# Optimization experiments

Hardware: AMD Instinct MI355X
Metric: run time of the kernel (lower is better)

The kernel has to match this reference:

```python
import jax, jax.numpy as jnp
import numpy as np

N, IN, HID, OUT, HEADS, E = 50000, 256, 128, 128, 2, 800000
NEG_SLOPE = 0.2


def gat_conv(x, edge_src, edge_dst, W, att_src, att_dst, bias):
    # x: [N, F_in]; W: [F_in, H*C]; att_*: [H, C]; bias: [C]
    n = x.shape[0]
    H, C = att_src.shape
    xl = (x @ W).reshape(n, H, C)                       # [N, H, C]
    a_src = jnp.sum(xl * att_src, axis=-1)              # [N, H]
    a_dst = jnp.sum(xl * att_dst, axis=-1)              # [N, H]
    e = jax.nn.leaky_relu(a_src[edge_src] + a_dst[edge_dst], NEG_SLOPE)  # [E+N, H]
    e_max = jax.ops.segment_max(e, edge_dst, num_segments=n)            # [N, H]
    e = jnp.exp(e - e_max[edge_dst])
    denom = jax.ops.segment_sum(e, edge_dst, num_segments=n)            # [N, H]
    alpha = e / (denom[edge_dst] + 1e-16)                               # [E+N, H]
    msg = xl[edge_src] * alpha[:, :, None]                              # [E+N, H, C]
    out = jax.ops.segment_sum(msg, edge_dst, num_segments=n)            # [N, H, C]
    return out.mean(axis=1) + bias                                      # concat=False: head mean


def setup_inputs() -> dict:
    key = jax.random.key(0)
    ks = jax.random.split(key, 12)
    x = jax.random.normal(ks[0], (N, IN), dtype=jnp.float32)
    edge_index = jax.random.randint(ks[1], (2, E), 0, N, dtype=jnp.int64)
    s = 0.1
    W0 = jax.random.normal(ks[2], (IN, HEADS * HID), dtype=jnp.float32) * s
    att_src0 = jax.random.normal(ks[3], (HEADS, HID), dtype=jnp.float32) * s
    att_dst0 = jax.random.normal(ks[4], (HEADS, HID), dtype=jnp.float32) * s
    bias0 = jnp.zeros((HID,), dtype=jnp.float32)
    W1 = jax.random.normal(ks[5], (HID, HEADS * HID), dtype=jnp.float32) * s
    att_src1 = jax.random.normal(ks[6], (HEADS, HID), dtype=jnp.float32) * s
    att_dst1 = jax.random.normal(ks[7], (HEADS, HID), dtype=jnp.float32) * s
    bias1 = jnp.zeros((HID,), dtype=jnp.float32)
    proj_w = jax.random.normal(ks[8], (HID, OUT), dtype=jnp.float32) * s
    proj_b = jnp.zeros((OUT,), dtype=jnp.float32)
    return {"x": x, "edge_index": edge_index,
            "W0": W0, "att_src0": att_src0, "att_dst0": att_dst0, "bias0": bias0,
            "W1": W1, "att_src1": att_src1, "att_dst1": att_dst1, "bias1": bias1,
            "proj_w": proj_w, "proj_b": proj_b}


def reference(x, edge_index, W0, att_src0, att_dst0, bias0, W1, att_src1, att_dst1, bias1, proj_w, proj_b):
    n = x.shape[0]
    loops = jnp.arange(n, dtype=edge_index.dtype)
    # PyG GATConv default add_self_loops=True
    src = jnp.concatenate([edge_index[0], loops])
    dst = jnp.concatenate([edge_index[1], loops])
    h = gat_conv(x, src, dst, W0, att_src0, att_dst0, bias0)
    h = jax.nn.gelu(h, approximate=False)
    h = gat_conv(h, src, dst, W1, att_src1, att_dst1, bias1)
    h = jax.nn.gelu(h, approximate=False)
    return h @ proj_w + proj_b
```

## Files before the change

### kernel.cpp

```cpp
#include <hip/hip_runtime.h>
#include <hip/hip_fp16.h>
#include <math.h>


#define NEG_SLOPE 0.2f

typedef __attribute__((ext_vector_type(8))) _Float16 f16x8;
typedef __attribute__((ext_vector_type(8))) ushort u16x8;
typedef __attribute__((ext_vector_type(4))) float f32x4;

__device__ __forceinline__ ushort f32_to_f16u(float x)
{
    return __half_as_ushort(__float2half(x));
}

__device__ __forceinline__ float f16u_to_f32(ushort u)
{
    return __half2float(__ushort_as_half(u));
}

__device__ __forceinline__ void split_f16(float x, ushort& h, ushort& l)
{
    const __half hh = __float2half(x);
    h = __half_as_ushort(hh);
    l = __half_as_ushort(__float2half(x - __half2float(hh)));
}

__device__ __forceinline__ float lrelu(float x)
{
    return x > 0.f ? x : NEG_SLOPE * x;
}

__device__ __forceinline__ float gelu_exact(float x)
{
    return 0.5f * x * (1.0f + erff(x * 0.7071067811865476f));
}

__global__ __launch_bounds__(256)
void prep_kernel(const float* __restrict__ W0, const float* __restrict__ W1,
                 const float* __restrict__ PW,
                 const float* __restrict__ as0, const float* __restrict__ ad0,
                 const float* __restrict__ as1, const float* __restrict__ ad1,
                 ushort* __restrict__ w0h, ushort* __restrict__ w0l,
                 ushort* __restrict__ w1h, ushort* __restrict__ w1l,
                 ushort* __restrict__ pwh, ushort* __restrict__ pwl,
                 float* __restrict__ wtd0, float* __restrict__ wt1,
                 int* __restrict__ cnt, int N)
{
    const int blk = blockIdx.x;
    if (blk >= 577) {
        int t2 = (blk - 577) * 256 + threadIdx.x;
        if (t2 < N) cnt[t2] = 0;
        return;
    }
    if (blk == 576) {
        const int col = threadIdx.x;
        float4 o;
        if (col < 128) o = make_float4(as0[col], 0.f, ad0[col], 0.f);
        else           o = make_float4(0.f, as0[col], 0.f, ad0[col]);
        *(float4*)(wtd0 + col * 4) = o;
        return;
    }
    if (blk < 448) {
        int t = blk * 256 + threadIdx.x;
        ushort h, l;
        if (t < 65536) {
            int k = t >> 8, n = t & 255;
            split_f16(W0[t], h, l);
            w0h[n * 256 + k] = h; w0l[n * 256 + k] = l;
        } else if (t < 65536 + 32768) {
            int u = t - 65536;
            int k = u >> 8, n = u & 255;
            split_f16(W1[u], h, l);
            w1h[n * 128 + k] = h; w1l[n * 128 + k] = l;
        } else {
            int u = t - 65536 - 32768;
            int k = u >> 7, n = u & 127;
            split_f16(PW[u], h, l);
            pwh[n * 128 + k] = h; pwl[n * 128 + k] = l;
        }
        return;
    }
    const int k = blk - 448;
    const int t = threadIdx.x;
    const int h = t >> 7, c = t & 127;
    const int lane = t & 63, wid = t >> 6;
    const float w = W1[(size_t)k * 256 + h * 128 + c];
    float ps = w * as1[h * 128 + c];
    float pd = w * ad1[h * 128 + c];
#pragma unroll
    for (int off = 1; off < 64; off <<= 1) {
        ps += __shfl_xor(ps, off, 64);
        pd += __shfl_xor(pd, off, 64);
    }
    __shared__ float sm[4][2];
    if (lane == 0) { sm[wid][0] = ps; sm[wid][1] = pd; }
    __syncthreads();
    if (t == 0) {
        wt1[k * 4 + 0] = sm[0][0] + sm[1][0];
        wt1[k * 4 + 1] = sm[2][0] + sm[3][0];
        wt1[k * 4 + 2] = sm[0][1] + sm[1][1];
        wt1[k * 4 + 3] = sm[2][1] + sm[3][1];
    }
}

template<int BN, bool SPLITA>
__global__ __launch_bounds__(512)
void mfma_gemm3(const float* __restrict__ Af,
                const ushort* __restrict__ A16,
                const ushort* __restrict__ Bth, const ushort* __restrict__ Btl,
                const float* __restrict__ bias,
                float* __restrict__ Cf, ushort* __restrict__ Cb,
                const float* __restrict__ watt,
                float* __restrict__ a_sc, float* __restrict__ a_dc,
                int M, int K)
{
    constexpr int NF = BN / 64;
    __shared__ ushort Ah[4][128][8];
    __shared__ ushort Bh[4][BN][8];
    __shared__ ushort Bl[4][BN][8];

    const int tid = threadIdx.x;
    const int r0 = blockIdx.x * 128;
    const int w = tid >> 6, lane = tid & 63;
    const int wr = (w & 1) * 64;
    const int wc = (w >> 1) * (BN / 4);
    const int lr = lane & 15, kb = lane >> 4;

    const int arow = tid >> 2;
    const int apl = tid & 3;

    f32x4 acc[4][NF] = {};

    for (int kk = 0; kk < K; kk += 32) {
        {
            const int row = r0 + arow;
            u16x8 h0 = {};
            if (row < M) {
                if constexpr (SPLITA) {
                    const float* p = Af + (size_t)row * K + kk + apl * 8;
                    float4 v0 = *(const float4*)(p);
                    float4 v1 = *(const float4*)(p + 4);
                    h0[0] = f32_to_f16u(v0.x); h0[1] = f32_to_f16u(v0.y);
                    h0[2] = f32_to_f16u(v0.z); h0[3] = f32_to_f16u(v0.w);
                    h0[4] = f32_to_f16u(v1.x); h0[5] = f32_to_f16u(v1.y);
                    h0[6] = f32_to_f16u(v1.z); h0[7] = f32_to_f16u(v1.w);
                } else {
                    h0 = *(const u16x8*)(A16 + (size_t)row * K + kk + apl * 8);
                }
            }
            *(u16x8*)&Ah[apl][arow][0] = h0;
        }
        if constexpr (BN == 256) {
            const int col = tid >> 1, half = tid & 1;
            const ushort* ph = Bth + (size_t)col * K + kk + half * 16;
            const ushort* pl = Btl + (size_t)col * K + kk + half * 16;
            *(u16x8*)&Bh[half * 2 + 0][col][0] = *(const u16x8*)(ph);
            *(u16x8*)&Bh[half * 2 + 1][col][0] = *(const u16x8*)(ph + 8);
            *(u16x8*)&Bl[half * 2 + 0][col][0] = *(const u16x8*)(pl);
            *(u16x8*)&Bl[half * 2 + 1][col][0] = *(const u16x8*)(pl + 8);
        } else {
            const int col = tid >> 2, pl = tid & 3;
            *(u16x8*)&Bh[pl][col][0] = *(const u16x8*)(Bth + (size_t)col * K + kk + pl * 8);
            *(u16x8*)&Bl[pl][col][0] = *(const u16x8*)(Btl + (size_t)col * K + kk + pl * 8);
        }
        __syncthreads();

        f16x8 ah[4];
#pragma unroll
        for (int m = 0; m < 4; ++m)
            ah[m] = *(const f16x8*)&Ah[kb][wr + m * 16 + lr][0];
#pragma unroll
        for (int n = 0; n < NF; ++n) {
            const f16x8 bh = *(const f16x8*)&Bh[kb][wc + n * 16 + lr][0];
            const f16x8 bl = *(const f16x8*)&Bl[kb][wc + n * 16 + lr][0];
#pragma unroll
            for (int m = 0; m < 4; ++m) {
                acc[m][n] = __builtin_amdgcn_mfma_f32_16x16x32_f16(ah[m], bh, acc[m][n], 0, 0, 0);
                acc[m][n] = __builtin_amdgcn_mfma_f32_16x16x32_f16(ah[m], bl, acc[m][n], 0, 0, 0);
            }
        }
        __syncthreads();
    }

#pragma unroll
    for (int n = 0; n < NF; ++n) {
        const int col = wc + n * 16 + lr;
        const float bv = bias ? bias[col] : 0.f;
#pragma unroll
        for (int m = 0; m < 4; ++m) {
            const int rowb = r0 + wr + m * 16 + kb * 4;
#pragma unroll
            for (int j = 0; j < 4; ++j) {
                const int row = rowb + j;
                if (row < M) {
                    const float val = acc[m][n][j] + bv;
                    if (Cf) Cf[(size_t)row * BN + col] = val;
                    if (Cb) Cb[(size_t)row * BN + col] = f32_to_f16u(val);
                }
            }
        }
    }

    if (watt) {
        float* sp = (float*)&Ah[0][0][0];
        float4 wv[NF];
#pragma unroll
        for (int n = 0; n < NF; ++n)
            wv[n] = *(const float4*)(watt + (wc + n * 16 + lr) * 4);
#pragma unroll
        for (int m = 0; m < 4; ++m) {
#pragma unroll
            for (int j = 0; j < 4; ++j) {
                float s0 = 0.f, s1 = 0.f, s2 = 0.f, s3 = 0.f;
#pragma unroll
                for (int n = 0; n < NF; ++n) {
                    const float v = acc[m][n][j];
                    s0 += v * wv[n].x;
                    s1 += v * wv[n].y;
                    s2 += v * wv[n].z;
                    s3 += v * wv[n].w;
                }
#pragma unroll
                for (int off = 1; off < 16; off <<= 1) {
                    s0 += __shfl_xor(s0, off, 64);
                    s1 += __shfl_xor(s1, off, 64);
                    s2 += __shfl_xor(s2, off, 64);
                    s3 += __shfl_xor(s3, off, 64);
                }
                if (lr == 0) {
                    const int row = wr + m * 16 + kb * 4 + j;
                    float* d = sp + ((w >> 1) * 128 + row) * 4;
                    d[0] = s0; d[1] = s1; d[2] = s2; d[3] = s3;
                }
            }
        }
        __syncthreads();
        const int row = tid >> 2, comp = tid & 3;
        const float s = sp[(0 * 128 + row) * 4 + comp]
                      + sp[(1 * 128 + row) * 4 + comp]
                      + sp[(2 * 128 + row) * 4 + comp]
                      + sp[(3 * 128 + row) * 4 + comp];
        const int gr = r0 + row;
        if (gr < M) {
            if (comp < 2) a_sc[(size_t)gr * 2 + comp] = s;
            else          a_dc[(size_t)gr * 2 + (comp - 2)] = s;
        }
    }
}

__global__ __launch_bounds__(256)
void gat_gather_kernel(const ushort* __restrict__ xlb,
                       const int* __restrict__ rowptr,
                       const int* __restrict__ esrc,
                       const float* __restrict__ a_si,
                       const float* __restrict__ a_di,
                       const float* __restrict__ bias,
                       const float* __restrict__ watt,
                       float* __restrict__ a_so, float* __restrict__ a_do,
                       ushort* __restrict__ outh,
                       int n)
{
    const int wave = threadIdx.x >> 6;
    const int lane = threadIdx.x & 63;
    const int v = blockIdx.x * 4 + wave;
    if (v >= n) return;
    const int half = lane >> 5;
    const int il = lane & 31;
    const int ch8 = il << 3;
    const int hsel = il >> 4;

    const float2 advv = *(const float2*)(a_di + (size_t)v * 2);
    const float2 asvv = *(const float2*)(a_si + (size_t)v * 2);
    const float wself0 = __expf(lrelu(asvv.x + advv.x));
    const float wself1 = __expf(lrelu(asvv.y + advv.y));
    const float wselfh = hsel ? wself1 : wself0;

    const u16x8 xv = *(const u16x8*)(xlb + (size_t)v * 256 + ch8);
    float acc[8];
#pragma unroll
    for (int k = 0; k < 8; ++k)
        acc[k] = (half == 0) ? wselfh * f16u_to_f32(xv[k]) : 0.f;

    float ssum0 = (il == 0) ? wself0 : 0.f;
    float ssum1 = (il == 0) ? wself1 : 0.f;

    const int beg = rowptr[v], end = rowptr[v + 1];
    for (int i = beg; i < end; i += 32) {
        const int cnt = min(32, end - i);
        int myidx = 0;
        float myw0 = 0.f, myw1 = 0.f;
        if (il < cnt) {
            myidx = esrc[i + il];
            const float2 e = *(const float2*)(a_si + (size_t)myidx * 2);
            myw0 = __expf(lrelu(e.x + advv.x));
            myw1 = __expf(lrelu(e.y + advv.y));
        }
        ssum0 += myw0;
        ssum1 += myw1;
#pragma unroll 2
        for (int j = 0; j < cnt; j += 2) {
            const int jj = j + half;
            const int src = __shfl(myidx, jj, 32);
            const float w0 = __shfl(myw0, jj, 32);
            const float w1 = __shfl(myw1, jj, 32);
            const float wgt = hsel ? w1 : w0;
            const u16x8 xs = *(const u16x8*)(xlb + (size_t)src * 256 + ch8);
#pragma unroll
            for (int k = 0; k < 8; ++k)
                acc[k] += wgt * f16u_to_f32(xs[k]);
        }
    }

#pragma unroll
    for (int off = 1; off <= 16; off <<= 1) {
        ssum0 += __shfl_xor(ssum0, off, 64);
        ssum1 += __shfl_xor(ssum1, off, 64);
    }
    const float inv = 1.0f / ((hsel ? ssum1 : ssum0) + 1e-16f);

    float o[8];
#pragma unroll
    for (int k = 0; k < 8; ++k) {
        float a = acc[k] + __shfl_xor(acc[k], 32, 64);
        a *= inv;
        o[k] = 0.5f * (a + __shfl_xor(a, 16, 64));
    }

    if (il < 16) {
        const float4 bb0 = *(const float4*)(bias + ch8);
        const float4 bb1 = *(const float4*)(bias + ch8 + 4);
        o[0] = gelu_exact(o[0] + bb0.x);
        o[1] = gelu_exact(o[1] + bb0.y);
        o[2] = gelu_exact(o[2] + bb0.z);
        o[3] = gelu_exact(o[3] + bb0.w);
        o[4] = gelu_exact(o[4] + bb1.x);
        o[5] = gelu_exact(o[5] + bb1.y);
        o[6] = gelu_exact(o[6] + bb1.z);
        o[7] = gelu_exact(o[7] + bb1.w);

        if (watt) {
            float s0 = 0.f, s1 = 0.f, d0 = 0.f, d1 = 0.f;
#pragma unroll
            for (int k = 0; k < 8; ++k) {
                const float4 wv = *(const float4*)(watt + (ch8 + k) * 4);
                s0 += o[k] * wv.x;
                s1 += o[k] * wv.y;
                d0 += o[k] * wv.z;
                d1 += o[k] * wv.w;
            }
#pragma unroll
            for (int off = 1; off <= 8; off <<= 1) {
                s0 += __shfl_xor(s0, off, 64);
                s1 += __shfl_xor(s1, off, 64);
                d0 += __shfl_xor(d0, off, 64);
                d1 += __shfl_xor(d1, off, 64);
            }
            if (lane == 0) {
                *(float2*)(a_so + (size_t)v * 2) = make_float2(s0, s1);
                *(float2*)(a_do + (size_t)v * 2) = make_float2(d0, d1);
            }
        }

        if (half == 0) {
            u16x8 st;
#pragma unroll
            for (int k = 0; k < 8; ++k) st[k] = f32_to_f16u(o[k]);
            *(u16x8*)(outh + (size_t)v * 128 + ch8) = st;
        }
    }
}

__global__ __launch_bounds__(256)
void hist_kernel(const int* __restrict__ ei, int* __restrict__ cnt, int E)
{
    int e = blockIdx.x * 256 + threadIdx.x;
    if (e < E) atomicAdd(&cnt[ei[E + e]], 1);
}

__global__ __launch_bounds__(256)
void blocksum_kernel(const int* __restrict__ cnt, int* __restrict__ bsum, int n)
{
    __shared__ int sm[256];
    const int t = threadIdx.x;
    const int i = blockIdx.x * 256 + t;
    sm[t] = (i < n) ? cnt[i] : 0;
    __syncthreads();
#pragma unroll
    for (int off = 1; off < 256; off <<= 1) {
        int u = (t >= off) ? sm[t - off] : 0;
        __syncthreads();
        sm[t] += u;
        __syncthreads();
    }
    if (t == 255) bsum[blockIdx.x] = sm[255];
}

__global__ __launch_bounds__(256)
void scan_bsum_kernel(int* __restrict__ bsum, int nb, int* __restrict__ ptr, int n)
{
    __shared__ int sm[256];
    const int t = threadIdx.x;
    const int v = (t < nb) ? bsum[t] : 0;
    sm[t] = v;
    __syncthreads();
#pragma unroll
    for (int off = 1; off < 256; off <<= 1) {
        int u = (t >= off) ? sm[t - off] : 0;
        __syncthreads();
        sm[t] += u;
        __syncthreads();
    }
    if (t < nb) bsum[t] = sm[t] - v;
    if (t == 255) ptr[n] = sm[255];
}

__global__ __launch_bounds__(256)
void scan_out_kernel(const int* __restrict__ cnt, const int* __restrict__ bsum,
                     int* __restrict__ ptr, int* __restrict__ pcur, int n)
{
    __shared__ int sm[256];
    const int t = threadIdx.x;
    const int i = blockIdx.x * 256 + t;
    const int v = (i < n) ? cnt[i] : 0;
    sm[t] = v;
    __syncthreads();
#pragma unroll
    for (int off = 1; off < 256; off <<= 1) {
        int u = (t >= off) ? sm[t - off] : 0;
        __syncthreads();
        sm[t] += u;
        __syncthreads();
    }
    if (i < n) {
        const int val = bsum[blockIdx.x] + sm[t] - v;
        ptr[i] = val;
        pcur[i] = val;
    }
}

__global__ __launch_bounds__(256)
void scatter_kernel(const int* __restrict__ ei, int* __restrict__ pcur,
                    int* __restrict__ esrc, int E)
{
    int e = blockIdx.x * 256 + threadIdx.x;
    if (e < E) {
        int dst = ei[E + e];
        int src = ei[e];
        int pos = atomicAdd(&pcur[dst], 1);
        esrc[pos] = src;
    }
}

extern "C" void kernel_launch(void* const* d_in, const int* in_sizes, int n_in,
                              void* d_out, int out_size, void* d_ws, size_t ws_size,
                              hipStream_t stream)
{
    const float* x       = (const float*)d_in[0];
    const int*   ei      = (const int*)d_in[1];
    const float* W0      = (const float*)d_in[2];
    const float* att_s0  = (const float*)d_in[3];
    const float* att_d0  = (const float*)d_in[4];
    const float* b0      = (const float*)d_in[5];
    const float* W1      = (const float*)d_in[6];
    const float* att_s1  = (const float*)d_in[7];
    const float* att_d1  = (const float*)d_in[8];
    const float* b1      = (const float*)d_in[9];
    const float* pw      = (const float*)d_in[10];
    const float* pb      = (const float*)d_in[11];

    const int N = in_sizes[0] / 256;
    const int E = in_sizes[1] / 2;
    const int NB = (N + 255) / 256;

    ushort* xlb  = (ushort*)d_ws;
    ushort* hbuf = xlb + (size_t)N * 256;
    float*  a_s  = (float*)(hbuf + (size_t)N * 128);
    float*  a_d  = a_s + (size_t)N * 2;
    float*  a_s2 = a_d + (size_t)N * 2;
    float*  a_d2 = a_s2 + (size_t)N * 2;
    float*  wtd0 = a_d2 + (size_t)N * 2;
    float*  wt1  = wtd0 + 256 * 4;
    int*    cnt  = (int*)(wt1 + 128 * 4);
    int*    ptr  = cnt + N;
    int*    pcur = ptr + (N + 1);
    int*    bsm  = pcur + N;
    int*    esr  = bsm + 256;
    ushort* w0h  = (ushort*)(esr + E);
    ushort* w0l  = w0h + 256 * 256;
    ushort* w1h  = w0l + 256 * 256;
    ushort* w1l  = w1h + 256 * 128;
    ushort* pwh  = w1l + 256 * 128;
    ushort* pwl  = pwh + 128 * 128;

    const int ablk = (N + 3) / 4;
    const int eblk = (E + 255) / 256;
    const int gblk = (N + 127) / 128;

    prep_kernel<<<577 + NB, 256, 0, stream>>>(
        W0, W1, pw, att_s0, att_d0, att_s1, att_d1,
        w0h, w0l, w1h, w1l, pwh, pwl, wtd0, wt1, cnt, N);

    hist_kernel<<<eblk, 256, 0, stream>>>(ei, cnt, E);
    blocksum_kernel<<<NB, 256, 0, stream>>>(cnt, bsm, N);
    scan_bsum_kernel<<<1, 256, 0, stream>>>(bsm, NB, ptr, N);
    scan_out_kernel<<<NB, 256, 0, stream>>>(cnt, bsm, ptr, pcur, N);
    scatter_kernel<<<eblk, 256, 0, stream>>>(ei, pcur, esr, E);

    mfma_gemm3<256, true><<<gblk, 512, 0, stream>>>(
        x, nullptr, w0h, w0l, nullptr, nullptr, xlb, wtd0, a_s, a_d, N, 256);
    gat_gather_kernel<<<ablk, 256, 0, stream>>>(
        xlb, ptr, esr, a_s, a_d, b0, wt1, a_s2, a_d2, hbuf, N);

    mfma_gemm3<256, false><<<gblk, 512, 0, stream>>>(
        nullptr, hbuf, w1h, w1l, nullptr, nullptr, xlb, nullptr, nullptr, nullptr, N, 128);
    gat_gather_kernel<<<ablk, 256, 0, stream>>>(
        xlb, ptr, esr, a_s2, a_d2, b1, nullptr, nullptr, nullptr, hbuf, N);

    mfma_gemm3<128, false><<<gblk, 512, 0, stream>>>(
        nullptr, hbuf, pwh, pwl, pb, (float*)d_out, nullptr, nullptr, nullptr, nullptr, N, 128);
}
```

Before: 325.6 us.

## Use direct global-to-LDS loads in GEMM and stage f16 output through LDS

Replaces the register-staged loads of the fp16 A and split B tiles with global_load_lds direct-to-LDS transfers, flattening the shared-memory layout to match the per-wave contiguous write pattern. The fp16 output path now goes through LDS so rows are written to global memory as coalesced 16-byte vectors instead of scattered 2-byte stores. This reduces VGPR pressure and store transactions, at the cost of extra barriers in the epilogue. The fp16 output path also drops the bias add, which changes behaviour if a bias were ever passed with Cb.

```diff
diff --git a/kernel.cpp b/kernel.cpp
--- a/kernel.cpp
+++ b/kernel.cpp
@@ -34,6 +34,13 @@
 __device__ __forceinline__ float gelu_exact(float x)
 {
     return 0.5f * x * (1.0f + erff(x * 0.7071067811865476f));
+}
+
+__device__ __forceinline__ void gload_lds16(const void* g, void* l)
+{
+    __builtin_amdgcn_global_load_lds(
+        (const __attribute__((address_space(1))) void*)g,
+        (__attribute__((address_space(3))) void*)l, 16, 0, 0);
 }
 
 __global__ __launch_bounds__(256)
@@ -116,9 +123,12 @@
                 int M, int K)
 {
     constexpr int NF = BN / 64;
-    __shared__ ushort Ah[4][128][8];
-    __shared__ ushort Bh[4][BN][8];
-    __shared__ ushort Bl[4][BN][8];
+    constexpr int ASZ = 4096;
+    constexpr int BSZ = BN * 32;
+    __shared__ ushort smem[ASZ + 2 * BSZ];
+    ushort* Ah = smem;
+    ushort* Bh = smem + ASZ;
+    ushort* Bl = smem + ASZ + BSZ;
 
     const int tid = threadIdx.x;
     const int r0 = blockIdx.x * 128;
@@ -127,53 +137,49 @@
     const int wc = (w >> 1) * (BN / 4);
     const int lr = lane & 15, kb = lane >> 4;
 
-    const int arow = tid >> 2;
-    const int apl = tid & 3;
+    const int a_apl = tid >> 7, a_row = tid & 127;
+    const int ca_row = min(r0 + a_row, M - 1);
+    const int arow_m = tid >> 2, apl_m = tid & 3;
 
     f32x4 acc[4][NF] = {};
 
     for (int kk = 0; kk < K; kk += 32) {
-        {
-            const int row = r0 + arow;
+        if constexpr (SPLITA) {
+            const int row = r0 + arow_m;
             u16x8 h0 = {};
             if (row < M) {
-                if constexpr (SPLITA) {
-                    const float* p = Af + (size_t)row * K + kk + apl * 8;
-                    float4 v0 = *(const float4*)(p);
-                    float4 v1 = *(const float4*)(p + 4);
-                    h0[0] = f32_to_f16u(v0.x); h0[1] = f32_to_f16u(v0.y);
-                    h0[2] = f32_to_f16u(v0.z); h0[3] = f32_to_f16u(v0.w);
-                    h0[4] = f32_to_f16u(v1.x); h0[5] = f32_to_f16u(v1.y);
-                    h0[6] = f32_to_f16u(v1.z); h0[7] = f32_to_f16u(v1.w);
-                } else {
-                    h0 = *(const u16x8*)(A16 + (size_t)row * K + kk + apl * 8);
-                }
-            }
-            *(u16x8*)&Ah[apl][arow][0] = h0;
-        }
-        if constexpr (BN == 256) {
-            const int col = tid >> 1, half = tid & 1;
-            const ushort* ph = Bth + (size_t)col * K + kk + half * 16;
-            const ushort* pl = Btl + (size_t)col * K + kk + half * 16;
-            *(u16x8*)&Bh[half * 2 + 0][col][0] = *(const u16x8*)(ph);
-            *(u16x8*)&Bh[half * 2 + 1][col][0] = *(const u16x8*)(ph + 8);
-            *(u16x8*)&Bl[half * 2 + 0][col][0] = *(const u16x8*)(pl);
-            *(u16x8*)&Bl[half * 2 + 1][col][0] = *(const u16x8*)(pl + 8);
+                const float* p = Af + (size_t)row * K + kk + apl_m * 8;
+                float4 v0 = *(const float4*)(p);
+                float4 v1 = *(const float4*)(p + 4);
+                h0[0] = f32_to_f16u(v0.x); h0[1] = f32_to_f16u(v0.y);
+                h0[2] = f32_to_f16u(v0.z); h0[3] = f32_to_f16u(v0.w);
+                h0[4] = f32_to_f16u(v1.x); h0[5] = f32_to_f16u(v1.y);
+                h0[6] = f32_to_f16u(v1.z); h0[7] = f32_to_f16u(v1.w);
+            }
+            *(u16x8*)&Ah[(apl_m * 128 + arow_m) * 8] = h0;
         } else {
-            const int col = tid >> 2, pl = tid & 3;
-            *(u16x8*)&Bh[pl][col][0] = *(const u16x8*)(Bth + (size_t)col * K + kk + pl * 8);
-            *(u16x8*)&Bl[pl][col][0] = *(const u16x8*)(Btl + (size_t)col * K + kk + pl * 8);
+            gload_lds16(A16 + (size_t)ca_row * K + kk + a_apl * 8,
+                        &Ah[(size_t)(w * 64) * 8]);
+        }
+#pragma unroll
+        for (int q = 0; q < (4 * BN) / 512; ++q) {
+            const int s = tid + q * 512;
+            const int pl = s / BN, col = s % BN;
+            const size_t goff = (size_t)col * K + kk + pl * 8;
+            const size_t lbase = (size_t)(w * 64 + q * 512) * 8;
+            gload_lds16(Bth + goff, &Bh[lbase]);
+            gload_lds16(Btl + goff, &Bl[lbase]);
         }
         __syncthreads();
 
         f16x8 ah[4];
 #pragma unroll
         for (int m = 0; m < 4; ++m)
-            ah[m] = *(const f16x8*)&Ah[kb][wr + m * 16 + lr][0];
+            ah[m] = *(const f16x8*)&Ah[(kb * 128 + wr + m * 16 + lr) * 8];
 #pragma unroll
         for (int n = 0; n < NF; ++n) {
-            const f16x8 bh = *(const f16x8*)&Bh[kb][wc + n * 16 + lr][0];
-            const f16x8 bl = *(const f16x8*)&Bl[kb][wc + n * 16 + lr][0];
+            const f16x8 bh = *(const f16x8*)&Bh[(kb * BN + wc + n * 16 + lr) * 8];
+            const f16x8 bl = *(const f16x8*)&Bl[(kb * BN + wc + n * 16 + lr) * 8];
 #pragma unroll
             for (int m = 0; m < 4; ++m) {
                 acc[m][n] = __builtin_amdgcn_mfma_f32_16x16x32_f16(ah[m], bh, acc[m][n], 0, 0, 0);
@@ -183,27 +189,54 @@
         __syncthreads();
     }
 
-#pragma unroll
-    for (int n = 0; n < NF; ++n) {
-        const int col = wc + n * 16 + lr;
-        const float bv = bias ? bias[col] : 0.f;
-#pragma unroll
-        for (int m = 0; m < 4; ++m) {
-            const int rowb = r0 + wr + m * 16 + kb * 4;
-#pragma unroll
-            for (int j = 0; j < 4; ++j) {
-                const int row = rowb + j;
-                if (row < M) {
-                    const float val = acc[m][n][j] + bv;
-                    if (Cf) Cf[(size_t)row * BN + col] = val;
-                    if (Cb) Cb[(size_t)row * BN + col] = f32_to_f16u(val);
+    if (Cb) {
+#pragma unroll
+        for (int c = 0; c < 2; ++c) {
+            if (wr == c * 64) {
+#pragma unroll
+                for (int n = 0; n < NF; ++n) {
+                    const int col = wc + n * 16 + lr;
+#pragma unroll
+                    for (int m = 0; m < 4; ++m) {
+                        const int rl = m * 16 + kb * 4;
+#pragma unroll
+                        for (int j = 0; j < 4; ++j)
+                            smem[(rl + j) * BN + col] = f32_to_f16u(acc[m][n][j]);
+                    }
                 }
             }
+            __syncthreads();
+#pragma unroll
+            for (int q = 0; q < BN / 64; ++q) {
+                const int slot = tid + q * 512;
+                const int row = c * 64 + (slot * 8) / BN;
+                const int colb = (slot * 8) % BN;
+                const int grow = r0 + row;
+                if (grow < M)
+                    *(u16x8*)(Cb + (size_t)grow * BN + colb) = *(const u16x8*)&smem[slot * 8];
+            }
+            __syncthreads();
+        }
+    }
+    if (Cf) {
+#pragma unroll
+        for (int n = 0; n < NF; ++n) {
+            const int col = wc + n * 16 + lr;
+            const float bv = bias ? bias[col] : 0.f;
+#pragma unroll
+            for (int m = 0; m < 4; ++m) {
+                const int rowb = r0 + wr + m * 16 + kb * 4;
+#pragma unroll
+                for (int j = 0; j < 4; ++j) {
+                    const int row = rowb + j;
+                    if (row < M) Cf[(size_t)row * BN + col] = acc[m][n][j] + bv;
+                }
+            }
         }
     }
 
     if (watt) {
-        float* sp = (float*)&Ah[0][0][0];
+        float* sp = (float*)smem;
         float4 wv[NF];
 #pragma unroll
         for (int n = 0; n < NF; ++n)
```

Result: slower. 355.9 us (+9.3%).
